# Kernel optimization log

Hardware: AMD Instinct MI355X
Metric: run time of the kernel (lower is better)

## Reference

```python
import jax, jax.numpy as jnp
import numpy as np

B, T, F = 2048, 60, 89
H = 1024
OUT = 30  # output_predicted_chords


def setup_inputs() -> dict:
    key = jax.random.key(0)
    k1, k2, k3, k4 = jax.random.split(key, 4)
    # small init scale keeps the relu-activated recurrence numerically stable
    s = 0.02
    return {
        "x": jax.random.normal(k1, (B, T, F), dtype=jnp.float32),
        "W": jax.random.normal(k2, (F, 4 * H), dtype=jnp.float32) * s,
        "U": jax.random.normal(k3, (H, 4 * H), dtype=jnp.float32) * s,
        "b": jnp.zeros((4 * H,), dtype=jnp.float32),
        "Wd": jax.random.normal(k4, (H, OUT), dtype=jnp.float32) * s,
        "bd": jnp.zeros((OUT,), dtype=jnp.float32),
    }


def _lstm_last_h(x, W, U, b):
    """Keras LSTM(activation='relu', recurrent_activation='sigmoid').
    Gate order in Keras kernels: i, f, c (candidate), o.
    Returns last hidden state h_T of shape [B, H]."""
    Bsz = x.shape[0]
    Hdim = U.shape[0]
    # precompute input projections for all timesteps: [T, B, 4H]
    xz = jnp.einsum('btf,fg->tbg', x, W) + b

    def step(carry, xz_t):
        h, c = carry
        z = xz_t + h @ U                      # [B, 4H]
        i, f, g, o = jnp.split(z, 4, axis=-1)
        i = jax.nn.sigmoid(i)
        f = jax.nn.sigmoid(f)
        g = jax.nn.relu(g)                    # activation='relu' on candidate
        o = jax.nn.sigmoid(o)
        c = f * c + i * g
        h = o * jax.nn.relu(c)                # activation='relu' on cell output
        return (h, c), None

    h0 = jnp.zeros((Bsz, Hdim), dtype=x.dtype)
    c0 = jnp.zeros((Bsz, Hdim), dtype=x.dtype)
    (hT, _), _ = jax.lax.scan(step, (h0, c0), xz)
    return hT


def reference(x, W, U, b, Wd, bd):
    # LSTM(return_sequences=True) then take x[:, -1, :] == last hidden state
    hT = _lstm_last_h(x, W, U, b)             # [B, H]
    y = hT @ Wd + bd                           # [B, OUT]
    return y.reshape(-1, OUT, 1)               # [B, 30, 1]
```

## Files before the change

kernel.cpp:

```cpp
#include <hip/hip_runtime.h>
#include <cstdint>
#include <cstddef>

#define Bsz 2048
#define Tseq 60
#define Fin 89
#define Hd 1024
#define G4 4096
#define KXP 128
#define NOUT 30

typedef _Float16 half8 __attribute__((ext_vector_type(8)));
typedef float f32x4 __attribute__((ext_vector_type(4)));

__device__ __forceinline__ void gload_lds16(const void* g, void* l) {
  __builtin_amdgcn_global_load_lds((const __attribute__((address_space(1))) void*)g,
                                   (__attribute__((address_space(3))) void*)l,
                                   16, 0, 0);
}

__device__ __forceinline__ float sigmoidf_fast(float x) {
  return 1.0f / (1.0f + __expf(-x));
}


__global__ __launch_bounds__(256) void convert_x(const float* __restrict__ x,
                                                 _Float16* __restrict__ xp) {
  int idx = blockIdx.x * 256 + threadIdx.x;
  int k = idx % KXP;
  int b = (idx / KXP) % Bsz;
  int t = idx / (KXP * Bsz);
  float v = (k < Fin) ? x[((size_t)b * Tseq + t) * Fin + k] : 0.0f;
  xp[idx] = (_Float16)v;
}

__global__ __launch_bounds__(256) void transpose_W(const float* __restrict__ W,
                                                   _Float16* __restrict__ Wpt) {
  __shared__ float tile[32][33];
  int n0 = blockIdx.x * 32;
  int k0 = blockIdx.y * 32;
  int tx = threadIdx.x, ty = threadIdx.y;
  for (int i = ty; i < 32; i += 8) {
    int k = k0 + i;
    tile[i][tx] = (k < Fin) ? W[(size_t)k * G4 + n0 + tx] : 0.0f;
  }
  __syncthreads();
  for (int i = ty; i < 32; i += 8)
    Wpt[(size_t)(n0 + i) * KXP + k0 + tx] = (_Float16)tile[tx][i];
}

__global__ __launch_bounds__(256) void transpose_U(const float* __restrict__ U,
                                                   _Float16* __restrict__ Upt) {
  __shared__ float tile[32][33];
  int n0 = blockIdx.x * 32;
  int k0 = blockIdx.y * 32;
  int tx = threadIdx.x, ty = threadIdx.y;
  for (int i = ty; i < 32; i += 8)
    tile[i][tx] = U[(size_t)(k0 + i) * G4 + n0 + tx];
  __syncthreads();
  for (int i = ty; i < 32; i += 8)
    Upt[(size_t)(n0 + i) * Hd + k0 + tx] = (_Float16)tile[tx][i];
}

__global__ __launch_bounds__(256, 2) void lstm_step(
    const _Float16* __restrict__ xp_t,
    const _Float16* __restrict__ Wpt,
    const _Float16* __restrict__ Upt,
    const float*    __restrict__ bias,
    const _Float16* __restrict__ h_in,
    _Float16*       __restrict__ h_out,
    float*          __restrict__ cst,
    int skip_h)
{
  __shared__ __align__(16) _Float16 As[2 * 8192];
  __shared__ __align__(16) _Float16 Bs[2 * 8192];

  const int tid  = threadIdx.x;
  const int wave = tid >> 6;
  const int lane = tid & 63;
  const int quad = lane >> 4;
  const int l16  = lane & 15;

  const int id   = blockIdx.x;
  const int virt = (id & 7) * 64 + (id >> 3);
  const int m0 = (virt & 15) * 128;
  const int j0 = (virt >> 4) * 32;

  const int srow = lane >> 2;
  const int qg   = (lane & 3) ^ ((lane >> 3) & 3);
  const int sA   = quad ^ ((l16 >> 1) & 3);

  const int hb    = 16 * (wave & 1);
  const int mwave = 64 * (wave >> 1);
  const int j  = j0 + hb + l16;
  const int uA = 4 * (wave >> 1);
  const int uB = wave & 1;
  const int aoff = l16 * 32 + sA * 8;

  float bv[4];
  for (int p = 0; p < 4; ++p) bv[p] = bias[p * Hd + j];

  f32x4 acc[4][4];
  for (int mi = 0; mi < 4; ++mi)
    for (int p = 0; p < 4; ++p)
      acc[mi][p] = f32x4{bv[p], bv[p], bv[p], bv[p]};

  auto stage = [&](int buf, int r) {
    const _Float16* Ab; const _Float16* Bb; int strA, strB, k0;
    if (r < 2) { Ab = xp_t; strA = KXP; Bb = Wpt; strB = KXP; k0 = r * 64; }
    else       { Ab = h_in; strA = Hd;  Bb = Upt; strB = Hd;  k0 = (r - 2) * 64; }
    _Float16* Ad = &As[buf * 8192];
    _Float16* Bd = &Bs[buf * 8192];
#pragma unroll
    for (int ii = 0; ii < 4; ++ii) {
      int i = ii * 4 + wave;
      int st = i >> 3, ci = i & 7;
      gload_lds16(Ab + (size_t)(m0 + ci * 16 + srow) * strA + k0 + st * 32 + qg * 8,
                  Ad + st * 4096 + ci * 512);
    }
#pragma unroll
    for (int ii = 0; ii < 4; ++ii) {
      int i = ii * 4 + wave;
      int st = i >> 3, ci = i & 7;
      int ln = ci * 16 + srow;
      int gn = (ln >> 5) * Hd + j0 + (ln & 31);
      gload_lds16(Bb + (size_t)gn * strB + k0 + st * 32 + qg * 8,
                  Bd + st * 4096 + ci * 512);
    }
  };

  auto compute = [&](int buf) {
#pragma unroll
    for (int st = 0; st < 2; ++st) {
      half8 a[4], bq[4];
      for (int mi = 0; mi < 4; ++mi)
        a[mi] = *(const half8*)&As[buf * 8192 + st * 4096 + (uA + mi) * 512 + aoff];
      for (int p = 0; p < 4; ++p)
        bq[p] = *(const half8*)&Bs[buf * 8192 + st * 4096 + (2 * p + uB) * 512 + aoff];
      for (int mi = 0; mi < 4; ++mi)
        for (int p = 0; p < 4; ++p)
          acc[mi][p] = __builtin_amdgcn_mfma_f32_16x16x32_f16(a[mi], bq[p],
                                                              acc[mi][p],
                                                              0, 0, 0);
    }
  };

  const int NR = skip_h ? 2 : 18;

  stage(0, 0);
  stage(1, 1);
  for (int r = 0; r < NR; ++r) {
    const int cur = r & 1;
    if (r < NR - 1) {
      asm volatile("s_waitcnt vmcnt(8)" ::: "memory");
    } else {
      asm volatile("s_waitcnt vmcnt(0)" ::: "memory");
    }
    __builtin_amdgcn_sched_barrier(0);
    __builtin_amdgcn_s_barrier();
    __builtin_amdgcn_s_setprio(1);
    compute(cur);
    __builtin_amdgcn_s_setprio(0);
    asm volatile("s_waitcnt lgkmcnt(0)" ::: "memory");
    __builtin_amdgcn_sched_barrier(0);
    __builtin_amdgcn_s_barrier();
    if (r + 2 < NR) stage(cur, r + 2);
  }

  for (int mi = 0; mi < 4; ++mi) {
    for (int r = 0; r < 4; ++r) {
      int row = m0 + mwave + mi * 16 + quad * 4 + r;
      size_t idx = (size_t)row * Hd + j;
      float iv = sigmoidf_fast(acc[mi][0][r]);
      float fv = sigmoidf_fast(acc[mi][1][r]);
      float gv = fmaxf(acc[mi][2][r], 0.0f);
      float ov = sigmoidf_fast(acc[mi][3][r]);
      float cprev = skip_h ? 0.0f : cst[idx];
      float cv = fv * cprev + iv * gv;
      cst[idx] = cv;
      float hv = ov * fmaxf(cv, 0.0f);
      h_out[idx] = (_Float16)hv;
    }
  }
}

__global__ __launch_bounds__(256) void final_dense(const _Float16* __restrict__ h,
                                                   const float* __restrict__ Wd,
                                                   const float* __restrict__ bd,
                                                   float* __restrict__ y) {
  __shared__ float hs[Hd];
  __shared__ float red[8][32];
  int bi = blockIdx.x;
  for (int k = threadIdx.x; k < Hd; k += 256)
    hs[k] = (float)h[(size_t)bi * Hd + k];
  __syncthreads();
  int o  = threadIdx.x & 31;
  int ch = threadIdx.x >> 5;
  float p = 0.0f;
  if (o < NOUT) {
    int k0 = ch * (Hd / 8);
    for (int k = k0; k < k0 + (Hd / 8); ++k)
      p += hs[k] * Wd[(size_t)k * NOUT + o];
  }
  red[ch][o] = p;
  __syncthreads();
  if (threadIdx.x < NOUT) {
    float s = bd[threadIdx.x];
    for (int c2 = 0; c2 < 8; ++c2) s += red[c2][threadIdx.x];
    y[(size_t)bi * NOUT + threadIdx.x] = s;
  }
}


extern "C" void kernel_launch(void* const* d_in, const int* in_sizes, int n_in,
                              void* d_out, int out_size, void* d_ws, size_t ws_size,
                              hipStream_t stream) {
  const float* x  = (const float*)d_in[0];
  const float* W  = (const float*)d_in[1];
  const float* U  = (const float*)d_in[2];
  const float* b  = (const float*)d_in[3];
  const float* Wd = (const float*)d_in[4];
  const float* bd = (const float*)d_in[5];
  float* y = (float*)d_out;

  char* ws = (char*)d_ws;
  _Float16* xp  = (_Float16*)ws; ws += (size_t)Tseq * Bsz * KXP * 2;
  _Float16* Wpt = (_Float16*)ws; ws += (size_t)G4 * KXP * 2;
  _Float16* Upt = (_Float16*)ws; ws += (size_t)G4 * Hd * 2;
  _Float16* hb0 = (_Float16*)ws; ws += (size_t)Bsz * Hd * 2;
  _Float16* hb1 = (_Float16*)ws; ws += (size_t)Bsz * Hd * 2;
  float*    cst = (float*)ws;    ws += (size_t)Bsz * Hd * 4;

  convert_x<<<(Tseq * Bsz * KXP) / 256, 256, 0, stream>>>(x, xp);
  transpose_W<<<dim3(G4 / 32, KXP / 32), dim3(32, 8), 0, stream>>>(W, Wpt);
  transpose_U<<<dim3(G4 / 32, Hd / 32), dim3(32, 8), 0, stream>>>(U, Upt);

  for (int t = 0; t < Tseq; ++t) {
    const _Float16* hin  = ((t - 1) & 1) ? hb1 : hb0;
    _Float16*       hout = (t & 1) ? hb1 : hb0;
    lstm_step<<<dim3((Bsz / 128) * (G4 / 128)), 256, 0, stream>>>(
        xp + (size_t)t * (Bsz * KXP), Wpt, Upt, b,
        (t == 0) ? hb0 : hin, hout, cst, (t == 0) ? 1 : 0);
  }

  final_dense<<<Bsz, 256, 0, stream>>>(hb1, Wd, bd, y);
}
```

Before: 1.760 ms.

## Load A operand directly into registers, keep only B in LDS

New measurement: 2.906 ms. 1.65x slower.

```diff
diff --git a/kernel.cpp b/kernel.cpp
--- a/kernel.cpp
+++ b/kernel.cpp
@@ -72,7 +72,6 @@
     float*          __restrict__ cst,
     int skip_h)
 {
-  __shared__ __align__(16) _Float16 As[2 * 8192];
   __shared__ __align__(16) _Float16 Bs[2 * 8192];
 
   const int tid  = threadIdx.x;
@@ -105,19 +104,11 @@
     for (int p = 0; p < 4; ++p)
       acc[mi][p] = f32x4{bv[p], bv[p], bv[p], bv[p]};
 
-  auto stage = [&](int buf, int r) {
-    const _Float16* Ab; const _Float16* Bb; int strA, strB, k0;
-    if (r < 2) { Ab = xp_t; strA = KXP; Bb = Wpt; strB = KXP; k0 = r * 64; }
-    else       { Ab = h_in; strA = Hd;  Bb = Upt; strB = Hd;  k0 = (r - 2) * 64; }
-    _Float16* Ad = &As[buf * 8192];
+  auto stageB = [&](int buf, int r) {
+    const _Float16* Bb; int strB, k0;
+    if (r < 2) { Bb = Wpt; strB = KXP; k0 = r * 64; }
+    else       { Bb = Upt; strB = Hd;  k0 = (r - 2) * 64; }
     _Float16* Bd = &Bs[buf * 8192];
-#pragma unroll
-    for (int ii = 0; ii < 4; ++ii) {
-      int i = ii * 4 + wave;
-      int st = i >> 3, ci = i & 7;
-      gload_lds16(Ab + (size_t)(m0 + ci * 16 + srow) * strA + k0 + st * 32 + qg * 8,
-                  Ad + st * 4096 + ci * 512);
-    }
 #pragma unroll
     for (int ii = 0; ii < 4; ++ii) {
       int i = ii * 4 + wave;
@@ -129,42 +120,65 @@
     }
   };
 
-  auto compute = [&](int buf) {
-#pragma unroll
-    for (int st = 0; st < 2; ++st) {
-      half8 a[4], bq[4];
+  auto loadA = [&](half8 (&ar)[8], int r) {
+    const _Float16* Ab; int strA, k0;
+    if (r < 2) { Ab = xp_t; strA = KXP; k0 = r * 64; }
+    else       { Ab = h_in; strA = Hd;  k0 = (r - 2) * 64; }
+    const _Float16* base = Ab + (size_t)(m0 + uA * 16 + l16) * strA + k0 + quad * 8;
+#pragma unroll
+    for (int mi = 0; mi < 4; ++mi)
+#pragma unroll
+      for (int st = 0; st < 2; ++st)
+        ar[mi * 2 + st] = *(const half8*)(base + (size_t)mi * 16 * strA + st * 32);
+  };
+
+  auto computeC = [&](const half8 (&ar)[8], int buf) {
+    const __attribute__((address_space(3))) _Float16* bs3 =
+        (const __attribute__((address_space(3))) _Float16*)&Bs[buf * 8192];
+    half8 bq[8];
+#pragma unroll
+    for (int st = 0; st < 2; ++st)
+#pragma unroll
+      for (int p = 0; p < 4; ++p)
+        asm volatile("ds_read_b128 %0, %1"
+                     : "=v"(bq[st * 4 + p])
+                     : "v"(bs3 + st * 4096 + (2 * p + uB) * 512 + aoff)
+                     : "memory");
+    asm volatile("s_waitcnt lgkmcnt(0)" ::: "memory");
+    __builtin_amdgcn_sched_barrier(0);
+#pragma unroll
+    for (int st = 0; st < 2; ++st)
+#pragma unroll
       for (int mi = 0; mi < 4; ++mi)
-        a[mi] = *(const half8*)&As[buf * 8192 + st * 4096 + (uA + mi) * 512 + aoff];
-      for (int p = 0; p < 4; ++p)
-        bq[p] = *(const half8*)&Bs[buf * 8192 + st * 4096 + (2 * p + uB) * 512 + aoff];
-      for (int mi = 0; mi < 4; ++mi)
+#pragma unroll
         for (int p = 0; p < 4; ++p)
-          acc[mi][p] = __builtin_amdgcn_mfma_f32_16x16x32_f16(a[mi], bq[p],
-                                                              acc[mi][p],
-                                                              0, 0, 0);
-    }
+          acc[mi][p] = __builtin_amdgcn_mfma_f32_16x16x32_f16(
+              ar[mi * 2 + st], bq[st * 4 + p], acc[mi][p], 0, 0, 0);
   };
 
   const int NR = skip_h ? 2 : 18;
 
-  stage(0, 0);
-  stage(1, 1);
-  for (int r = 0; r < NR; ++r) {
-    const int cur = r & 1;
-    if (r < NR - 1) {
-      asm volatile("s_waitcnt vmcnt(8)" ::: "memory");
-    } else {
-      asm volatile("s_waitcnt vmcnt(0)" ::: "memory");
-    }
+  stageB(0, 0);
+  half8 arA[8], arB[8];
+  loadA(arA, 0);
+  stageB(1, 1);
+
+  auto iter = [&](int r, int buf, const half8 (&acur)[8], half8 (&anxt)[8]) {
+    if (r < NR - 1) asm volatile("s_waitcnt vmcnt(12)" ::: "memory");
+    else            asm volatile("s_waitcnt vmcnt(0)"  ::: "memory");
     __builtin_amdgcn_sched_barrier(0);
     __builtin_amdgcn_s_barrier();
+    if (r + 1 < NR) loadA(anxt, r + 1);
     __builtin_amdgcn_s_setprio(1);
-    compute(cur);
+    computeC(acur, buf);
     __builtin_amdgcn_s_setprio(0);
-    asm volatile("s_waitcnt lgkmcnt(0)" ::: "memory");
-    __builtin_amdgcn_sched_barrier(0);
     __builtin_amdgcn_s_barrier();
-    if (r + 2 < NR) stage(cur, r + 2);
+    if (r + 2 < NR) stageB(buf, r + 2);
+  };
+
+  for (int r = 0; r < NR; r += 2) {
+    iter(r,     0, arA, arB);
+    iter(r + 1, 1, arB, arA);
   }
 
   for (int mi = 0; mi < 4; ++mi) {
```
